# Optimization experiments

Hardware: AMD Instinct MI355X
Metric: run time of the kernel (lower is better)

## Reference

```python
import jax, jax.numpy as jnp
import numpy as np

B, M, N = 32, 16, 256        # problems, constraints, items
P = M * N                    # nodes per problem graph (4096)
NODES = B * P                # 131072
E = 2_097_152                # edges (avg degree 16)
F_IN = 16
H = 128                      # n_hidden[0..5], n_hidden[7]
H6 = 256                     # n_hidden[6]


def setup_inputs() -> dict:
    key = jax.random.key(0)
    ks = jax.random.split(key, 24)
    nrm = lambda k, shape: jax.random.normal(k, shape, jnp.float32) * 0.05
    inp = {}
    inp["G"] = jax.random.normal(ks[0], (NODES, F_IN), jnp.float32)
    inp["edge_index"] = jax.random.randint(ks[1], (2, E), 0, NODES)
    inp["edge_weight"] = jax.random.uniform(ks[2], (E,), jnp.float32)
    inp["edge_attribute"] = jax.random.normal(ks[3], (E, 1), jnp.float32)  # unused, kept for API parity
    inp["value_var_solutions"] = jax.random.randint(ks[4], (B, P), 0, 2).astype(jnp.int32)
    inp["item_values"] = jax.random.uniform(ks[5], (B, N), jnp.float32)
    # learned parameters
    inp["W_emb1"], inp["b_emb1"] = nrm(ks[6], (F_IN, H)), jnp.zeros((H,), jnp.float32)
    inp["W_emb2"], inp["b_emb2"] = nrm(ks[7], (H, H)), jnp.zeros((H,), jnp.float32)
    for i, t in enumerate(("c1", "c2")):  # GatedGraphConv(H, num_layers=2) x2
        inp[f"{t}_W"]  = nrm(ks[8 + 3 * i], (2, H, H))
        inp[f"{t}_wi"] = nrm(ks[9 + 3 * i], (3 * H, H))
        inp[f"{t}_wh"] = nrm(ks[10 + 3 * i], (3 * H, H))
        inp[f"{t}_bi"] = jnp.zeros((3 * H,), jnp.float32)
        inp[f"{t}_bh"] = jnp.zeros((3 * H,), jnp.float32)
    inp["W_g1"], inp["b_g1"] = nrm(ks[14], (H, H)), jnp.zeros((H,), jnp.float32)
    inp["W_g2"], inp["b_g2"] = nrm(ks[15], (H, H)), jnp.zeros((H,), jnp.float32)
    inp["W_l1"], inp["b_l1"] = nrm(ks[16], (2 * H, H6)), jnp.zeros((H6,), jnp.float32)
    inp["W_l2"], inp["b_l2"] = nrm(ks[17], (H6, H)), jnp.zeros((H,), jnp.float32)
    inp["W_l3"], inp["b_l3"] = nrm(ks[18], (H, 1)), jnp.zeros((1,), jnp.float32)
    return inp


def _gru_cell(m, h, wi, wh, bi, bh):
    # torch.nn.GRUCell with gate order (r, z, n)
    gi = m @ wi.T + bi
    gh = h @ wh.T + bh
    ir, iz, inn = jnp.split(gi, 3, axis=-1)
    hr, hz, hn = jnp.split(gh, 3, axis=-1)
    r = jax.nn.sigmoid(ir + hr)
    z = jax.nn.sigmoid(iz + hz)
    n = jnp.tanh(inn + r * hn)
    return (1.0 - z) * n + z * h


def _gated_graph_conv(x, src, dst, ew, W, wi, wh, bi, bh):
    # PyG GatedGraphConv: for each layer, m_i = sum_{j->i} ew * (x_j @ W_l); x = GRU(m, x)
    nnodes = x.shape[0]
    for l in range(W.shape[0]):
        msg = (x @ W[l])[src] * ew[:, None]          # [E, H]
        agg = jax.ops.segment_sum(msg, dst, num_segments=nnodes)
        x = _gru_cell(agg, x, wi, wh, bi, bh)
    return x


def reference(G, edge_index, edge_weight, edge_attribute, value_var_solutions, item_values,
              W_emb1, b_emb1, W_emb2, b_emb2,
              c1_W, c1_wi, c1_wh, c1_bi, c1_bh,
              c2_W, c2_wi, c2_wh, c2_bi, c2_bh,
              W_g1, b_g1, W_g2, b_g2,
              W_l1, b_l1, W_l2, b_l2, W_l3, b_l3):
    src, dst = edge_index[0], edge_index[1]
    x = jax.nn.relu(G @ W_emb1 + b_emb1)
    x = jax.nn.relu(x @ W_emb2 + b_emb2)
    x = jax.nn.relu(_gated_graph_conv(x, src, dst, edge_weight, c1_W, c1_wi, c1_wh, c1_bi, c1_bh))
    x = jax.nn.relu(_gated_graph_conv(x, src, dst, edge_weight, c2_W, c2_wi, c2_wh, c2_bi, c2_bh))
    x = jax.nn.relu(x @ W_g1 + b_g1)
    x = x @ W_g2 + b_g2                              # [NODES, H]
    # ragged per-graph mean pool + broadcast-concat (all graphs same size -> reshape)
    xg = x.reshape(B, P, H)
    ge = xg.mean(axis=1, keepdims=True)              # [B, 1, H] graph embedding
    u = jnp.concatenate([xg, jnp.broadcast_to(ge, xg.shape)], axis=-1)  # [B, P, 2H]
    u = jax.nn.relu(u @ W_l1 + b_l1)
    u = jax.nn.relu(u @ W_l2 + b_l2)
    u = (u @ W_l3 + b_l3)[..., 0]                    # [B, P]
    # bound: dx[j,i] = sol[0,i] - sol[j,i]; bound = u.dx + sum_i val[i]*sol[0,i]
    sol = value_var_solutions.reshape(B, M, N).astype(u.dtype)
    dx = sol[:, :1, :] - sol                         # [B, M, N]
    bounds = (jnp.einsum('bp,bp->b', u, dx.reshape(B, P))
              + jnp.einsum('bn,bn->b', item_values, sol[:, 0, :]))
    return bounds
```

## Files before the change

### kernel.cpp

```cpp
#include <hip/hip_runtime.h>

#define NODES   131072
#define EDGES   2097152
#define H       128
#define NB      32
#define PP      4096

typedef short bf16x8 __attribute__((ext_vector_type(8)));
typedef float f32x4  __attribute__((ext_vector_type(4)));
typedef float f32x2  __attribute__((ext_vector_type(2)));
typedef unsigned short u16;

#define RZE 65536
#define AIE 16384
#define AHE 16384
#define LYRE (RZE + AIE + AHE)

#define CAPP 18432

__global__ __launch_bounds__(128) void gnn_pinit(int* __restrict__ pcur) {
  pcur[threadIdx.x] = threadIdx.x * CAPP;
}

#define B1_BLOCKS 256
#define B1_TILES  4
__global__ __launch_bounds__(256) void gnn_bin1(const int* __restrict__ src, const int* __restrict__ dst,
                                                const float* __restrict__ ew, int* __restrict__ pcur,
                                                uint2* __restrict__ stage) {
  __shared__ int hist[128];
  __shared__ int pbase[128];
  const int tid = threadIdx.x;
  for (int t = 0; t < B1_TILES; ++t) {
    if (tid < 128) hist[tid] = 0;
    __syncthreads();
    const int ebase = blockIdx.x * (B1_TILES * 2048) + t * 2048;
    int parts[8], ranks[8];
    uint2 recs[8];
#pragma unroll
    for (int i = 0; i < 8; ++i) {
      int e = ebase + i * 256 + tid;
      int d = dst[e];
      int s = src[e];
      float w = ew[e];
      int wq = (int)fminf(w * 32768.f + 0.5f, 32767.f);
      parts[i] = d >> 10;
      recs[i].x = ((unsigned)s << 15) | (unsigned)wq;
      recs[i].y = (unsigned)d;
      ranks[i] = atomicAdd(&hist[parts[i]], 1);
    }
    __syncthreads();
    if (tid < 128) {
      int c = hist[tid];
      pbase[tid] = c ? atomicAdd(&pcur[tid], c) : 0;
    }
    __syncthreads();
#pragma unroll
    for (int i = 0; i < 8; ++i)
      stage[pbase[parts[i]] + ranks[i]] = recs[i];
    __syncthreads();
  }
}

__global__ __launch_bounds__(256) void gnn_bin2(const uint2* __restrict__ stage,
                                                const int* __restrict__ pcur,
                                                int* __restrict__ rowptr,
                                                unsigned* __restrict__ epack) {
  __shared__ int h[1024];
  __shared__ int ws[256];
  __shared__ int pc[128];
  __shared__ int gb_s;
  const int tid = threadIdx.x;
  const int p = blockIdx.x;
  const int node0 = p << 10;
  const int s0 = p * CAPP;
  const int cnt = pcur[p] - s0;
#pragma unroll
  for (int i = 0; i < 4; ++i) h[i * 256 + tid] = 0;
  if (tid < 128) pc[tid] = pcur[tid] - tid * CAPP;
  __syncthreads();
  for (int r = tid; r < cnt; r += 256)
    atomicAdd(&h[(int)stage[s0 + r].y - node0], 1);
  if (tid == 0) {
    int s = 0;
    for (int i = 0; i < p; ++i) s += pc[i];
    gb_s = s;
  }
  __syncthreads();
  const int gbase = gb_s;
  int a0 = h[tid * 4 + 0], a1 = h[tid * 4 + 1], a2 = h[tid * 4 + 2], a3 = h[tid * 4 + 3];
  int s1 = a0 + a1, s2 = s1 + a2, s3 = s2 + a3;
  ws[tid] = s3;
  __syncthreads();
  for (int o = 1; o < 256; o <<= 1) {
    int u = (tid >= o) ? ws[tid - o] : 0;
    __syncthreads();
    ws[tid] += u;
    __syncthreads();
  }
  int eb = gbase + (tid ? ws[tid - 1] : 0);
  int4 rp;
  rp.x = eb; rp.y = eb + a0; rp.z = eb + s1; rp.w = eb + s2;
  *(int4*)(rowptr + node0 + tid * 4) = rp;
  h[tid * 4 + 0] = rp.x; h[tid * 4 + 1] = rp.y; h[tid * 4 + 2] = rp.z; h[tid * 4 + 3] = rp.w;
  if (p == 127 && tid == 255) rowptr[NODES] = EDGES;
  __syncthreads();
  for (int r = tid; r < cnt; r += 256) {
    uint2 q = stage[s0 + r];
    int pos = atomicAdd(&h[(int)q.y - node0], 1);
    epack[pos] = q.x;
  }
}

__device__ __forceinline__ unsigned gnn_pack2bf(float a, float b) {
  union { float f; unsigned u; } x, y; x.f = a; y.f = b;
  unsigned ua = (x.u + 0x7FFFu + ((x.u >> 16) & 1u)) >> 16;
  unsigned ub = (y.u + 0x7FFFu + ((y.u >> 16) & 1u)) >> 16;
  return ua | (ub << 16);
}

__device__ __forceinline__ u16 gnn_f2bf(float a) {
  union { float f; unsigned u; } x; x.f = a;
  return (u16)((x.u + 0x7FFFu + ((x.u >> 16) & 1u)) >> 16);
}

__device__ __forceinline__ float gnn_bf2f(u16 h) {
  union { unsigned u; float f; } x; x.u = ((unsigned)h) << 16; return x.f;
}

__device__ __forceinline__ unsigned char gnn_f2fp8(float v) {
  return (unsigned char)(__builtin_amdgcn_cvt_pk_fp8_f32(v, v, 0, false) & 0xFF);
}

template<bool HI>
__device__ __forceinline__ unsigned gnn_bf2fp8pk(unsigned pv, unsigned old) {
  union { unsigned u; float f; } lo, hi;
  lo.u = pv << 16; hi.u = pv & 0xFFFF0000u;
  return __builtin_amdgcn_cvt_pk_fp8_f32(lo.f, hi.f, old, HI);
}

__device__ __forceinline__ float gnn_sig(float x)  { return 1.f / (1.f + __expf(-x)); }
__device__ __forceinline__ float gnn_tanh(float x) { return 1.f - 2.f / (1.f + __expf(2.f * x)); }

__global__ __launch_bounds__(256) void gnn_agg(const unsigned char* __restrict__ X8,
                                               const int* __restrict__ rowptr,
                                               const unsigned* __restrict__ epack,
                                               u16* __restrict__ T) {
  const int tid = threadIdx.x;
  const int wave = tid >> 6, lane = tid & 63;
  const int g = lane >> 4, s = lane & 15;
  const unsigned soff = (unsigned)(s << 3);
  const int node = blockIdx.x * 16 + wave * 4 + g;
  const int e1 = rowptr[node + 1];
  const int e0 = rowptr[node];
  float acc[8];
#pragma unroll
  for (int c = 0; c < 8; ++c) acc[c] = 0.f;

  for (int it = e0; __any(it < e1); it += 8) {
    unsigned qv[8];
#pragma unroll
    for (int j = 0; j < 8; ++j) {
      int t = it + j;
      t = t < e1 ? t : e1 - 1;
      t = t < 0 ? 0 : t;
      qv[j] = epack[t];
    }
    uint2 pv[8];
#pragma unroll
    for (int j = 0; j < 8; ++j)
      pv[j] = *(const uint2*)(X8 + ((((qv[j] >> 15) << 7)) | soff));
#pragma unroll
    for (int j = 0; j < 8; ++j) {
      float w = (it + j) < e1 ? (float)(qv[j] & 0x7FFFu) : 0.f;
      f32x2 f01 = __builtin_amdgcn_cvt_pk_f32_fp8(pv[j].x, false);
      f32x2 f23 = __builtin_amdgcn_cvt_pk_f32_fp8(pv[j].x, true);
      f32x2 f45 = __builtin_amdgcn_cvt_pk_f32_fp8(pv[j].y, false);
      f32x2 f67 = __builtin_amdgcn_cvt_pk_f32_fp8(pv[j].y, true);
      acc[0] = fmaf(w, f01.x, acc[0]);  acc[1] = fmaf(w, f01.y, acc[1]);
      acc[2] = fmaf(w, f23.x, acc[2]);  acc[3] = fmaf(w, f23.y, acc[3]);
      acc[4] = fmaf(w, f45.x, acc[4]);  acc[5] = fmaf(w, f45.y, acc[5]);
      acc[6] = fmaf(w, f67.x, acc[6]);  acc[7] = fmaf(w, f67.y, acc[7]);
    }
  }

  const float sc = 1.f / 32768.f;
  uint4 o;
  o.x = gnn_pack2bf(acc[0] * sc, acc[1] * sc);
  o.y = gnn_pack2bf(acc[2] * sc, acc[3] * sc);
  o.z = gnn_pack2bf(acc[4] * sc, acc[5] * sc);
  o.w = gnn_pack2bf(acc[6] * sc, acc[7] * sc);
  *(uint4*)(T + (long)node * H + s * 8) = o;
}

__global__ __launch_bounds__(384) void gnn_prep(const float* __restrict__ c1W, const float* __restrict__ c1wi,
                                                const float* __restrict__ c2W, const float* __restrict__ c2wi,
                                                const float* __restrict__ wh1, const float* __restrict__ wh2,
                                                float* __restrict__ Wc, float* __restrict__ whT) {
  if (blockIdx.x < 512) {
    __shared__ float wrow[128];
    int l = blockIdx.x >> 7, k = blockIdx.x & 127, j = threadIdx.x;
    const float* Wl = (l < 2 ? c1W : c2W) + (l & 1) * 128 * 128;
    const float* wi = l < 2 ? c1wi : c2wi;
    if (j < 128) wrow[j] = Wl[k * 128 + j];
    __syncthreads();
    float acc = 0.f;
    for (int m = 0; m < 128; ++m) acc = fmaf(wrow[m], wi[j * 128 + m], acc);
    Wc[(long)l * 49152 + k * 384 + j] = acc;
  } else {
    int bb = blockIdx.x - 512;
    int c = bb >> 7, k = bb & 127, j = threadIdx.x;
    const float* wh = c ? wh2 : wh1;
    whT[((long)c * 128 + k) * 384 + j] = wh[j * 128 + k];
  }
}

template<int K>
__device__ __forceinline__ void gnn_stage_bf(const u16* __restrict__ A, long row0,
                                             u16* lds, int tid) {
  constexpr int CH = K / 8;
#pragma unroll
  for (int it = 0; it < (64 * CH) / 256; ++it) {
    int c = it * 256 + tid;
    int row = c / CH, ktq = c % CH;
    uint4 v = *(const uint4*)(A + (row0 + row) * K + ktq * 8);
    int slot = ktq * 64 + (row ^ (ktq & 7));
    *(uint4*)(lds + slot * 8) = v;
  }
}

template<int K>
__device__ __forceinline__ void gnn_stage32(const u16* __restrict__ A, long row0,
                                            u16* lds, int tid) {
  constexpr int CH = K / 8;
#pragma unroll
  for (int it = 0; it < (32 * CH) / 256; ++it) {
    int c = it * 256 + tid;
    int row = c / CH, ktq = c % CH;
    uint4 v = *(const uint4*)(A + (row0 + row) * K + ktq * 8);
    int slot = ktq * 32 + (row ^ (ktq & 7));
    *(uint4*)(lds + slot * 8) = v;
  }
}

__device__ __forceinline__ bf16x8 gnn_afrag(const u16* lds, int rt, int ktq, int l16) {
  int slot = ktq * 64 + ((rt * 16 + l16) ^ (ktq & 7));
  return *(const bf16x8*)(lds + slot * 8);
}

__device__ __forceinline__ bf16x8 gnn_afrag32(const u16* lds, int rt, int ktq, int l16) {
  int slot = ktq * 32 + ((rt * 16 + l16) ^ (ktq & 7));
  return *(const bf16x8*)(lds + slot * 8);
}

__device__ __forceinline__ bf16x8 gnn_bfrag(const u16* __restrict__ pk,
                                            int ct, int kt, int KT, int lane) {
  return *(const bf16x8*)(pk + (((long)(ct * KT + kt)) * 64 + lane) * 8);
}

__device__ __forceinline__ void gnn_lds_put(u16* lds, int row, int col, float v) {
  int kq = col >> 3, of = col & 7;
  lds[(kq * 64 + (row ^ (kq & 7))) * 8 + of] = gnn_f2bf(v);
}

__device__ __forceinline__ float gnn_lds_get(const u16* lds, int row, int col) {
  int kq = col >> 3, of = col & 7;
  return gnn_bf2f(lds[(kq * 64 + (row ^ (kq & 7))) * 8 + of]);
}

__device__ __forceinline__ float gnn_lds_get32(const u16* lds, int row, int col) {
  int kq = col >> 3, of = col & 7;
  return gnn_bf2f(lds[(kq * 32 + (row ^ (kq & 7))) * 8 + of]);
}

__device__ __forceinline__ void gnn_pack_body(const float* __restrict__ W0, const float* __restrict__ W1,
                                              int ksplit, int LD, int coff, int KT, int b, int lane,
                                              u16* __restrict__ dst) {
  int kt = b % KT, ct = b / KT;
  int col = ct * 16 + (lane & 15) + coff;
  int kb = kt * 32 + ((lane >> 4) & 3) * 8;
  u16 h[8];
#pragma unroll
  for (int j = 0; j < 8; ++j) {
    int k = kb + j;
    float v = (k < ksplit) ? W0[(long)k * LD + col] : W1[(long)(k - ksplit) * LD + col];
    h[j] = gnn_f2bf(v);
  }
  uint4 o;
  o.x = (unsigned)h[0] | ((unsigned)h[1] << 16);
  o.y = (unsigned)h[2] | ((unsigned)h[3] << 16);
  o.z = (unsigned)h[4] | ((unsigned)h[5] << 16);
  o.w = (unsigned)h[6] | ((unsigned)h[7] << 16);
  ((uint4*)dst)[(long)b * 64 + lane] = o;
}

__global__ __launch_bounds__(64) void gnn_pack(const float* __restrict__ Wc, const float* __restrict__ whT,
                                               const float* __restrict__ We2, const float* __restrict__ Wg1,
                                               const float* __restrict__ Wg2, const float* __restrict__ Wl1,
                                               const float* __restrict__ Wl2, u16* __restrict__ pk) {
  int lane = threadIdx.x;
  if (blockIdx.x < 768) {
    int l = blockIdx.x / 192, r = blockIdx.x % 192;
    const float* Wcl = Wc + (long)l * 49152;
    const float* whl = whT + (long)(l >> 1) * 49152;
    u16* base = pk + (long)l * LYRE;
    if (r < 128)      gnn_pack_body(Wcl, whl, 128, 384, 0,   8, r,       lane, base);
    else if (r < 160) gnn_pack_body(Wcl, Wcl, 128, 384, 256, 4, r - 128, lane, base + RZE);
    else              gnn_pack_body(whl, whl, 128, 384, 256, 4, r - 160, lane, base + RZE + AIE);
  } else {
    int b = blockIdx.x - 768;
    u16* pe2 = pk + 4 * LYRE;
    if (b < 32)       gnn_pack_body(We2, We2, 128, 128, 0, 4, b,       lane, pe2);
    else if (b < 64)  gnn_pack_body(Wg1, Wg1, 128, 128, 0, 4, b - 32,  lane, pe2 + 16384);
    else if (b < 96)  gnn_pack_body(Wg2, Wg2, 128, 128, 0, 4, b - 64,  lane, pe2 + 32768);
    else if (b < 160) gnn_pack_body(Wl1, Wl1, 128, 256, 0, 4, b - 96,  lane, pe2 + 49152);
    else              gnn_pack_body(Wl2, Wl2, 256, 128, 0, 8, b - 160, lane, pe2 + 81920);
  }
}

__global__ __launch_bounds__(256) void gnn_emb(const float* __restrict__ G, const float* __restrict__ W1,
                                               const float* __restrict__ b1,
                                               const u16* __restrict__ pk2, const float* __restrict__ b2,
                                               u16* __restrict__ C, unsigned char* __restrict__ C8) {
  __shared__ u16 As[64 * 128];
  __shared__ float AsT[16][68];
  __shared__ float Ws[16][132];
  const int tid = threadIdx.x;
  const int lane = tid & 63, wave = tid >> 6;
  const int quad = lane >> 4, l16 = lane & 15;
  const long row0 = (long)blockIdx.x * 64;

  {
    const int lr  = tid >> 2;
    const int lk4 = (tid & 3) * 4;
    const int wk  = tid >> 4;
    const int wj4 = (tid & 15) * 4;
    float4 a = *(const float4*)(G + (row0 + lr) * 16 + lk4);
    AsT[lk4 + 0][lr] = a.x; AsT[lk4 + 1][lr] = a.y; AsT[lk4 + 2][lr] = a.z; AsT[lk4 + 3][lr] = a.w;
    float4 w0 = *(const float4*)(W1 + (long)wk * 128 + wj4);
    float4 w1 = *(const float4*)(W1 + (long)wk * 128 + 64 + wj4);
    *(float4*)(&Ws[wk][wj4]) = w0;
    *(float4*)(&Ws[wk][64 + wj4]) = w1;
    __syncthreads();

    const int tx = tid & 15, ty = tid >> 4;
    float acc0[16], acc1[16];
#pragma unroll
    for (int i = 0; i < 16; ++i) { acc0[i] = 0.f; acc1[i] = 0.f; }
#pragma unroll
    for (int k = 0; k < 16; ++k) {
      float4 av  = *(const float4*)(&AsT[k][ty * 4]);
      float4 wv0 = *(const float4*)(&Ws[k][tx * 4]);
      float4 wv1 = *(const float4*)(&Ws[k][64 + tx * 4]);
#pragma unroll
      for (int i = 0; i < 4; ++i) {
        float av_i = (i == 0) ? av.x : (i == 1) ? av.y : (i == 2) ? av.z : av.w;
        acc0[i * 4 + 0] = fmaf(av_i, wv0.x, acc0[i * 4 + 0]);
        acc0[i * 4 + 1] = fmaf(av_i, wv0.y, acc0[i * 4 + 1]);
        acc0[i * 4 + 2] = fmaf(av_i, wv0.z, acc0[i * 4 + 2]);
        acc0[i * 4 + 3] = fmaf(av_i, wv0.w, acc0[i * 4 + 3]);
        acc1[i * 4 + 0] = fmaf(av_i, wv1.x, acc1[i * 4 + 0]);
        acc1[i * 4 + 1] = fmaf(av_i, wv1.y, acc1[i * 4 + 1]);
        acc1[i * 4 + 2] = fmaf(av_i, wv1.z, acc1[i * 4 + 2]);
        acc1[i * 4 + 3] = fmaf(av_i, wv1.w, acc1[i * 4 + 3]);
      }
    }
#pragma unroll
    for (int i = 0; i < 4; ++i) {
      int row = ty * 4 + i;
#pragma unroll
      for (int j = 0; j < 4; ++j) {
        int c0 = tx * 4 + j;
        gnn_lds_put(As, row, c0,      fmaxf(acc0[i * 4 + j] + b1[c0], 0.f));
        gnn_lds_put(As, row, c0 + 64, fmaxf(acc1[i * 4 + j] + b1[c0 + 64], 0.f));
      }
    }
  }
  __syncthreads();

  f32x4 zero4 = {0.f, 0.f, 0.f, 0.f};
  f32x4 acc[4][2];
#pragma unroll
  for (int rt = 0; rt < 4; ++rt)
#pragma unroll
    for (int ct = 0; ct < 2; ++ct) acc[rt][ct] = zero4;
#pragma unroll
  for (int kt = 0; kt < 4; ++kt) {
    int ktq = kt * 4 + quad;
    bf16x8 af[4];
#pragma unroll
    for (int rt = 0; rt < 4; ++rt) af[rt] = gnn_afrag(As, rt, ktq, l16);
#pragma unroll
    for (int ct = 0; ct < 2; ++ct) {
      bf16x8 bf = gnn_bfrag(pk2, wave * 2 + ct, kt, 4, lane);
#pragma unroll
      for (int rt = 0; rt < 4; ++rt)
        acc[rt][ct] = __builtin_amdgcn_mfma_f32_16x16x32_bf16(af[rt], bf, acc[rt][ct], 0, 0, 0);
    }
  }
#pragma unroll
  for (int ct = 0; ct < 2; ++ct) {
    int col = (wave * 2 + ct) * 16 + l16;
    float bv = b2[col];
#pragma unroll
    for (int rt = 0; rt < 4; ++rt) {
      long row = row0 + rt * 16 + quad * 4;
#pragma unroll
      for (int r = 0; r < 4; ++r) {
        float v = fmaxf(acc[rt][ct][r] + bv, 0.f);
        C[(row + r) * H + col] = gnn_f2bf(v);
        C8[(row + r) * H + col] = gnn_f2fp8(v);
      }
    }
  }
}

#define OSTR 136

template<int RELU>
__global__ __launch_bounds__(256, 3) void gnn_mgru(const u16* __restrict__ T, const u16* __restrict__ X,
                                                   const u16* __restrict__ pkRZ,
                                                   const u16* __restrict__ pkAI,
                                                   const u16* __restrict__ pkAH,
                                                   const float* __restrict__ bi, const float* __restrict__ bh,
                                                   u16* __restrict__ Y,
                                                   unsigned char* __restrict__ Y8) {
  __shared__ u16 Ts[32 * OSTR];
  __shared__ u16 Xs[32 * 128];
  const int tid = threadIdx.x;
  const int lane = tid & 63, wave = tid >> 6;
  const int quad = lane >> 4, l16 = lane & 15;
  const long row0 = (long)blockIdx.x * 32;
  gnn_stage32<128>(T, row0, Ts, tid);
  gnn_stage32<128>(X, row0, Xs, tid);

  float brz[2], bzz[2], bin_[2], bhn[2];
#pragma unroll
  for (int c = 0; c < 2; ++c) {
    int col = (wave * 2 + c) * 16 + l16;
    brz[c]  = bi[col] + bh[col];
    bzz[c]  = bi[128 + col] + bh[128 + col];
    bin_[c] = bi[256 + col];
    bhn[c]  = bh[256 + col];
  }
  __syncthreads();

  f32x4 zero4 = {0.f, 0.f, 0.f, 0.f};
  f32x4 g1[2][2], g2[2][2];

#pragma unroll
  for (int rt = 0; rt < 2; ++rt)
#pragma unroll
    for (int c = 0; c < 2; ++c) g1[rt][c] = zero4;
#pragma unroll
  for (int kt = 0; kt < 4; ++kt) {
    int ktq = kt * 4 + quad;
    bf16x8 tf[2], xf[2];
#pragma unroll
    for (int rt = 0; rt < 2; ++rt) { tf[rt] = gnn_afrag32(Ts, rt, ktq, l16); xf[rt] = gnn_afrag32(Xs, rt, ktq, l16); }
#pragma unroll
    for (int c = 0; c < 2; ++c) {
      int ct = wave * 2 + c;
      bf16x8 bRT = gnn_bfrag(pkRZ, ct, kt,     8, lane);
      bf16x8 bRX = gnn_bfrag(pkRZ, ct, kt + 4, 8, lane);
#pragma unroll
      for (int rt = 0; rt < 2; ++rt) {
        g1[rt][c] = __builtin_amdgcn_mfma_f32_16x16x32_bf16(tf[rt], bRT, g1[rt][c], 0, 0, 0);
        g1[rt][c] = __builtin_amdgcn_mfma_f32_16x16x32_bf16(xf[rt], bRX, g1[rt][c], 0, 0, 0);
      }
    }
  }
#pragma unroll
  for (int rt = 0; rt < 2; ++rt)
#pragma unroll
    for (int c = 0; c < 2; ++c)
#pragma unroll
      for (int r = 0; r < 4; ++r)
        g1[rt][c][r] = gnn_sig(g1[rt][c][r] + brz[c]);

#pragma unroll
  for (int rt = 0; rt < 2; ++rt)
#pragma unroll
    for (int c = 0; c < 2; ++c) g2[rt][c] = zero4;
#pragma unroll
  for (int kt = 0; kt < 4; ++kt) {
    int ktq = kt * 4 + quad;
    bf16x8 xf[2];
#pragma unroll
    for (int rt = 0; rt < 2; ++rt) xf[rt] = gnn_afrag32(Xs, rt, ktq, l16);
#pragma unroll
    for (int c = 0; c < 2; ++c) {
      bf16x8 bAH = gnn_bfrag(pkAH, wave * 2 + c, kt, 4, lane);
#pragma unroll
      for (int rt = 0; rt < 2; ++rt)
        g2[rt][c] = __builtin_amdgcn_mfma_f32_16x16x32_bf16(xf[rt], bAH, g2[rt][c], 0, 0, 0);
    }
  }
#pragma unroll
  for (int rt = 0; rt < 2; ++rt)
#pragma unroll
    for (int c = 0; c < 2; ++c)
#pragma unroll
      for (int r = 0; r < 4; ++r)
        g1[rt][c][r] = g1[rt][c][r] * (g2[rt][c][r] + bhn[c]);

#pragma unroll
  for (int rt = 0; rt < 2; ++rt)
#pragma unroll
    for (int c = 0; c < 2; ++c) g2[rt][c] = zero4;
#pragma unroll
  for (int kt = 0; kt < 4; ++kt) {
    int ktq = kt * 4 + quad;
    bf16x8 tf[2];
#pragma unroll
    for (int rt = 0; rt < 2; ++rt) tf[rt] = gnn_afrag32(Ts, rt, ktq, l16);
#pragma unroll
    for (int c = 0; c < 2; ++c) {
      bf16x8 bAI = gnn_bfrag(pkAI, wave * 2 + c, kt, 4, lane);
#pragma unroll
      for (int rt = 0; rt < 2; ++rt)
        g2[rt][c] = __builtin_amdgcn_mfma_f32_16x16x32_bf16(tf[rt], bAI, g2[rt][c], 0, 0, 0);
    }
  }
#pragma unroll
  for (int rt = 0; rt < 2; ++rt)
#pragma unroll
    for (int c = 0; c < 2; ++c)
#pragma unroll
      for (int r = 0; r < 4; ++r)
        g1[rt][c][r] = gnn_tanh(g2[rt][c][r] + bin_[c] + g1[rt][c][r]);

#pragma unroll
  for (int rt = 0; rt < 2; ++rt)
#pragma unroll
    for (int c = 0; c < 2; ++c) g2[rt][c] = zero4;
#pragma unroll
  for (int kt = 0; kt < 4; ++kt) {
    int ktq = kt * 4 + quad;
    bf16x8 tf[2], xf[2];
#pragma unroll
    for (int rt = 0; rt < 2; ++rt) { tf[rt] = gnn_afrag32(Ts, rt, ktq, l16); xf[rt] = gnn_afrag32(Xs, rt, ktq, l16); }
#pragma unroll
    for (int c = 0; c < 2; ++c) {
      int ct = wave * 2 + c;
      bf16x8 bZT = gnn_bfrag(pkRZ, 8 + ct, kt,     8, lane);
      bf16x8 bZX = gnn_bfrag(pkRZ, 8 + ct, kt + 4, 8, lane);
#pragma unroll
      for (int rt = 0; rt < 2; ++rt) {
        g2[rt][c] = __builtin_amdgcn_mfma_f32_16x16x32_bf16(tf[rt], bZT, g2[rt][c], 0, 0, 0);
        g2[rt][c] = __builtin_amdgcn_mfma_f32_16x16x32_bf16(xf[rt], bZX, g2[rt][c], 0, 0, 0);
      }
    }
  }

  float yv[2][2][4];
#pragma unroll
  for (int rt = 0; rt < 2; ++rt)
#pragma unroll
    for (int c = 0; c < 2; ++c) {
      int col = (wave * 2 + c) * 16 + l16;
      int rowl = rt * 16 + quad * 4;
#pragma unroll
      for (int r = 0; r < 4; ++r) {
        float z = gnn_sig(g2[rt][c][r] + bzz[c]);
        float h = gnn_lds_get32(Xs, rowl + r, col);
        float v = (1.f - z) * g1[rt][c][r] + z * h;
        if (RELU) v = fmaxf(v, 0.f);
        yv[rt][c][r] = v;
      }
    }
  __syncthreads();
#pragma unroll
  for (int rt = 0; rt < 2; ++rt)
#pragma unroll
    for (int c = 0; c < 2; ++c) {
      int col = (wave * 2 + c) * 16 + l16;
      int rowl = rt * 16 + quad * 4;
#pragma unroll
      for (int r = 0; r < 4; ++r)
        Ts[(rowl + r) * OSTR + col] = gnn_f2bf(yv[rt][c][r]);
    }
  __syncthreads();
  {
    const int orow = tid >> 3;
    const int oc = (tid & 7) * 16;
    const u16* src = Ts + orow * OSTR + oc;
    uint4 a = *(const uint4*)(src);
    uint4 b = *(const uint4*)(src + 8);
    u16* yd = Y + (row0 + orow) * H + oc;
    *(uint4*)(yd) = a;
    *(uint4*)(yd + 8) = b;
    if (Y8) {
      uint4 o8;
      o8.x = gnn_bf2fp8pk<true>(a.y, gnn_bf2fp8pk<false>(a.x, 0));
      o8.y = gnn_bf2fp8pk<true>(a.w, gnn_bf2fp8pk<false>(a.z, 0));
      o8.z = gnn_bf2fp8pk<true>(b.y, gnn_bf2fp8pk<false>(b.x, 0));
      o8.w = gnn_bf2fp8pk<true>(b.w, gnn_bf2fp8pk<false>(b.z, 0));
      *(uint4*)(Y8 + (row0 + orow) * H + oc) = o8;
    }
  }
}

__global__ __launch_bounds__(256) void gnn_g1g2(const u16* __restrict__ A,
                                                const u16* __restrict__ pk1, const float* __restrict__ b1,
                                                const u16* __restrict__ pk2, const float* __restrict__ b2,
                                                u16* __restrict__ C, float* __restrict__ ge) {
  __shared__ u16 As[64 * 128];
  __shared__ u16 Ys[64 * 128];
  const int tid = threadIdx.x;
  const int lane = tid & 63, wave = tid >> 6;
  const int quad = lane >> 4, l16 = lane & 15;
  const long row0 = (long)blockIdx.x * 64;
  gnn_stage_bf<128>(A, row0, As, tid);
  __syncthreads();

  f32x4 zero4 = {0.f, 0.f, 0.f, 0.f};
  f32x4 acc[4][2];
#pragma unroll
  for (int rt = 0; rt < 4; ++rt)
#pragma unroll
    for (int ct = 0; ct < 2; ++ct) acc[rt][ct] = zero4;
#pragma unroll
  for (int kt = 0; kt < 4; ++kt) {
    int ktq = kt * 4 + quad;
    bf16x8 af[4];
#pragma unroll
    for (int rt = 0; rt < 4; ++rt) af[rt] = gnn_afrag(As, rt, ktq, l16);
#pragma unroll
    for (int ct = 0; ct < 2; ++ct) {
      bf16x8 bf = gnn_bfrag(pk1, wave * 2 + ct, kt, 4, lane);
#pragma unroll
      for (int rt = 0; rt < 4; ++rt)
        acc[rt][ct] = __builtin_amdgcn_mfma_f32_16x16x32_bf16(af[rt], bf, acc[rt][ct], 0, 0, 0);
    }
  }
#pragma unroll
  for (int ct = 0; ct < 2; ++ct) {
    int col = (wave * 2 + ct) * 16 + l16;
    float bv = b1[col];
#pragma unroll
    for (int rt = 0; rt < 4; ++rt) {
      int rowl = rt * 16 + quad * 4;
#pragma unroll
      for (int r = 0; r < 4; ++r)
        gnn_lds_put(Ys, rowl + r, col, fmaxf(acc[rt][ct][r] + bv, 0.f));
    }
  }
  __syncthreads();

  f32x4 acc2[4][2];
#pragma unroll
  for (int rt = 0; rt < 4; ++rt)
#pragma unroll
    for (int ct = 0; ct < 2; ++ct) acc2[rt][ct] = zero4;
#pragma unroll
  for (int kt = 0; kt < 4; ++kt) {
    int ktq = kt * 4 + quad;
    bf16x8 af[4];
#pragma unroll
    for (int rt = 0; rt < 4; ++rt) af[rt] = gnn_afrag(Ys, rt, ktq, l16);
#pragma unroll
    for (int ct = 0; ct < 2; ++ct) {
      bf16x8 bf = gnn_bfrag(pk2, wave * 2 + ct, kt, 4, lane);
#pragma unroll
      for (int rt = 0; rt < 4; ++rt)
        acc2[rt][ct] = __builtin_amdgcn_mfma_f32_16x16x32_bf16(af[rt], bf, acc2[rt][ct], 0, 0, 0);
    }
  }
  float psum[2];
#pragma unroll
  for (int ct = 0; ct < 2; ++ct) {
    int col = (wave * 2 + ct) * 16 + l16;
    float bv = b2[col];
    float cs = 0.f;
#pragma unroll
    for (int rt = 0; rt < 4; ++rt) {
      long row = row0 + rt * 16 + quad * 4;
#pragma unroll
      for (int r = 0; r < 4; ++r) {
        float v = acc2[rt][ct][r] + bv;
        cs += v;
        C[(row + r) * H + col] = gnn_f2bf(v);
      }
    }
    psum[ct] = cs;
  }
  const int b = (int)(row0 >> 12);
#pragma unroll
  for (int ct = 0; ct < 2; ++ct) {
    float v = psum[ct];
    v += __shfl_xor(v, 16);
    v += __shfl_xor(v, 32);
    if (quad == 0) {
      int col = (wave * 2 + ct) * 16 + l16;
      atomicAdd(&ge[b * H + col], v);
    }
  }
}

__global__ __launch_bounds__(256) void gnn_l1l2(const u16* __restrict__ A,
                                                const u16* __restrict__ pk1, const float* __restrict__ gb,
                                                const u16* __restrict__ pk2, const float* __restrict__ b2,
                                                u16* __restrict__ C) {
  __shared__ u16 As[64 * 128];
  __shared__ u16 Us[64 * 256];
  const int tid = threadIdx.x;
  const int lane = tid & 63, wave = tid >> 6;
  const int quad = lane >> 4, l16 = lane & 15;
  const long row0 = (long)blockIdx.x * 64;
  gnn_stage_bf<128>(A, row0, As, tid);
  __syncthreads();

  f32x4 zero4 = {0.f, 0.f, 0.f, 0.f};
  {
    f32x4 acc[4][4];
#pragma unroll
    for (int rt = 0; rt < 4; ++rt)
#pragma unroll
      for (int ct = 0; ct < 4; ++ct) acc[rt][ct] = zero4;
#pragma unroll
    for (int kt = 0; kt < 4; ++kt) {
      int ktq = kt * 4 + quad;
      bf16x8 af[4];
#pragma unroll
      for (int rt = 0; rt < 4; ++rt) af[rt] = gnn_afrag(As, rt, ktq, l16);
#pragma unroll
      for (int ct = 0; ct < 4; ++ct) {
        bf16x8 bf = gnn_bfrag(pk1, wave * 4 + ct, kt, 4, lane);
#pragma unroll
        for (int rt = 0; rt < 4; ++rt)
          acc[rt][ct] = __builtin_amdgcn_mfma_f32_16x16x32_bf16(af[rt], bf, acc[rt][ct], 0, 0, 0);
      }
    }
    const float* bp = gb + (row0 >> 12) * 256;
#pragma unroll
    for (int ct = 0; ct < 4; ++ct) {
      int col = (wave * 4 + ct) * 16 + l16;
      float bv = bp[col];
#pragma unroll
      for (int rt = 0; rt < 4; ++rt) {
        int rowl = rt * 16 + quad * 4;
#pragma unroll
        for (int r = 0; r < 4; ++r)
          gnn_lds_put(Us, rowl + r, col, fmaxf(acc[rt][ct][r] + bv, 0.f));
      }
    }
  }
  __syncthreads();

  f32x4 acc2[4][2];
#pragma unroll
  for (int rt = 0; rt < 4; ++rt)
#pragma unroll
    for (int ct = 0; ct < 2; ++ct) acc2[rt][ct] = zero4;
#pragma unroll
  for (int kt = 0; kt < 8; ++kt) {
    int ktq = kt * 4 + quad;
    bf16x8 af[4];
#pragma unroll
    for (int rt = 0; rt < 4; ++rt) af[rt] = gnn_afrag(Us, rt, ktq, l16);
#pragma unroll
    for (int ct = 0; ct < 2; ++ct) {
      bf16x8 bf = gnn_bfrag(pk2, wave * 2 + ct, kt, 8, lane);
#pragma unroll
      for (int rt = 0; rt < 4; ++rt)
        acc2[rt][ct] = __builtin_amdgcn_mfma_f32_16x16x32_bf16(af[rt], bf, acc2[rt][ct], 0, 0, 0);
    }
  }
#pragma unroll
  for (int ct = 0; ct < 2; ++ct) {
    int col = (wave * 2 + ct) * 16 + l16;
    float bv = b2[col];
#pragma unroll
    for (int rt = 0; rt < 4; ++rt) {
      long row = row0 + rt * 16 + quad * 4;
#pragma unroll
      for (int r = 0; r < 4; ++r)
        C[(row + r) * H + col] = gnn_f2bf(fmaxf(acc2[rt][ct][r] + bv, 0.f));
    }
  }
}

__global__ __launch_bounds__(256) void gnn_gbias(const float* __restrict__ ge, const float* __restrict__ Wl1b,
                                                 const float* __restrict__ bl1, float* __restrict__ gb) {
  __shared__ float g[128];
  int b = blockIdx.x, t = threadIdx.x;
  if (t < 128) g[t] = ge[b * H + t] * (1.f / 4096.f);
  __syncthreads();
  float acc = bl1[t];
  for (int k = 0; k < 128; ++k) acc = fmaf(g[k], Wl1b[k * 256 + t], acc);
  gb[b * 256 + t] = acc;
}

__global__ __launch_bounds__(256) void gnn_item(const float* __restrict__ iv, const int* __restrict__ vvs,
                                                float* __restrict__ out) {
  __shared__ float s[256];
  int b = blockIdx.x, t = threadIdx.x;
  float v = iv[b * 256 + t] * (float)vvs[(long)b * PP + t];
  s[t] = v; __syncthreads();
  for (int off = 128; off > 0; off >>= 1) {
    if (t < off) s[t] += s[t + off];
    __syncthreads();
  }
  if (t == 0) out[b] = s[0];
}

__global__ __launch_bounds__(256) void gnn_bound(const u16* __restrict__ U2, const float* __restrict__ wl3,
                                                 const float* __restrict__ bl3, const int* __restrict__ vvs,
                                                 float* __restrict__ out) {
  int tid = threadIdx.x;
  int wave = tid >> 6, lane = tid & 63;
  int b = blockIdx.x >> 6;
  long node0 = (long)blockIdx.x * 64 + wave * 16;
  float w0 = wl3[lane * 2], w1 = wl3[lane * 2 + 1];
  float bl = bl3[0];
  float acc = 0.f;
  for (int i = 0; i < 16; ++i) {
    long node = node0 + i;
    unsigned pv = *(const unsigned*)(U2 + node * H + lane * 2);
    union { unsigned u; float f; } lo, hi;
    lo.u = pv << 16; hi.u = pv & 0xFFFF0000u;
    float p = lo.f * w0 + hi.f * w1;
#pragma unroll
    for (int off = 32; off > 0; off >>= 1) p += __shfl_down(p, off);
    if (lane == 0) {
      int pp = (int)(node & (PP - 1));
      int m = pp >> 8, n = pp & 255;
      if (m != 0) {
        float dx = (float)(vvs[((long)b << 12) + n] - vvs[((long)b << 12) + pp]);
        acc += (p + bl) * dx;
      }
    }
  }
  __shared__ float s[4];
  if (lane == 0) s[wave] = acc;
  __syncthreads();
  if (tid == 0) atomicAdd(&out[b], s[0] + s[1] + s[2] + s[3]);
}

extern "C" void kernel_launch(void* const* d_in, const int* in_sizes, int n_in,
                              void* d_out, int out_size, void* d_ws, size_t ws_size,
                              hipStream_t stream) {
  const float* G      = (const float*)d_in[0];
  const int*   ei     = (const int*)d_in[1];
  const int*   esrc   = ei;
  const int*   edst   = ei + EDGES;
  const float* ew     = (const float*)d_in[2];
  const int*   vvs    = (const int*)d_in[4];
  const float* iv     = (const float*)d_in[5];
  const float* W_emb1 = (const float*)d_in[6];
  const float* b_emb1 = (const float*)d_in[7];
  const float* W_emb2 = (const float*)d_in[8];
  const float* b_emb2 = (const float*)d_in[9];
  const float* c1_W   = (const float*)d_in[10];
  const float* c1_wi  = (const float*)d_in[11];
  const float* c1_wh  = (const float*)d_in[12];
  const float* c1_bi  = (const float*)d_in[13];
  const float* c1_bh  = (const float*)d_in[14];
  const float* c2_W   = (const float*)d_in[15];
  const float* c2_wi  = (const float*)d_in[16];
  const float* c2_wh  = (const float*)d_in[17];
  const float* c2_bi  = (const float*)d_in[18];
  const float* c2_bh  = (const float*)d_in[19];
  const float* W_g1   = (const float*)d_in[20];
  const float* b_g1   = (const float*)d_in[21];
  const float* W_g2   = (const float*)d_in[22];
  const float* b_g2   = (const float*)d_in[23];
  const float* W_l1   = (const float*)d_in[24];
  const float* b_l1   = (const float*)d_in[25];
  const float* W_l2   = (const float*)d_in[26];
  const float* b_l2   = (const float*)d_in[27];
  const float* W_l3   = (const float*)d_in[28];
  const float* b_l3   = (const float*)d_in[29];
  float* out = (float*)d_out;
  (void)in_sizes; (void)n_in; (void)out_size; (void)ws_size;

  char* wsb = (char*)d_ws;
  size_t off = 0;
  auto carve = [&](size_t bytes) -> char* {
    char* p = wsb + off;
    off += (bytes + 255) & ~(size_t)255;
    return p;
  };
  u16*   xa     = (u16*)carve(sizeof(u16) * (size_t)NODES * H);
  u16*   xc     = (u16*)carve(sizeof(u16) * (size_t)NODES * H);
  u16*   tb     = (u16*)carve(sizeof(u16) * (size_t)NODES * H);
  float* Wc     = (float*)carve(sizeof(float) * 4 * H * 384);
  float* whT    = (float*)carve(sizeof(float) * 2 * H * 384);
  u16*   pk     = (u16*)carve(sizeof(u16) * 507904);
  int*   rowptr = (int*)carve(sizeof(int) * (NODES + 1));
  int*   pcur   = (int*)carve(sizeof(int) * 128);
  uint2* stage  = (uint2*)carve(sizeof(uint2) * (size_t)128 * CAPP);
  unsigned* epack = (unsigned*)carve(sizeof(unsigned) * EDGES);
  float* ge     = (float*)carve(sizeof(float) * NB * H);
  float* gb     = (float*)carve(sizeof(float) * NB * 256);

  unsigned char* X8 = (unsigned char*)stage;

  u16* pkRZ[4]; u16* pkAI[4]; u16* pkAH[4];
  for (int l = 0; l < 4; ++l) {
    pkRZ[l] = pk + (long)l * LYRE;
    pkAI[l] = pk + (long)l * LYRE + RZE;
    pkAH[l] = pk + (long)l * LYRE + RZE + AIE;
  }
  u16* pe2 = pk + 4 * LYRE;
  u16* pg1 = pe2 + 16384;
  u16* pg2 = pe2 + 32768;
  u16* pl1 = pe2 + 49152;
  u16* pl2 = pe2 + 81920;

  hipMemsetAsync(ge, 0, sizeof(float) * NB * H, stream);
  gnn_pinit<<<1, 128, 0, stream>>>(pcur);
  gnn_bin1<<<B1_BLOCKS, 256, 0, stream>>>(esrc, edst, ew, pcur, stage);
  gnn_bin2<<<128, 256, 0, stream>>>(stage, pcur, rowptr, epack);

  gnn_prep<<<768, 384, 0, stream>>>(c1_W, c1_wi, c2_W, c2_wi, c1_wh, c2_wh, Wc, whT);
  gnn_pack<<<992, 64, 0, stream>>>(Wc, whT, W_emb2, W_g1, W_g2, W_l1, W_l2, pk);

  gnn_emb<<<NODES / 64, 256, 0, stream>>>(G, W_emb1, b_emb1, pe2, b_emb2, xc, X8);

  gnn_agg<<<NODES / 16, 256, 0, stream>>>(X8, rowptr, epack, tb);
  gnn_mgru<0><<<NODES / 32, 256, 0, stream>>>(tb, xc, pkRZ[0], pkAI[0], pkAH[0], c1_bi, c1_bh, xa, X8);
  gnn_agg<<<NODES / 16, 256, 0, stream>>>(X8, rowptr, epack, tb);
  gnn_mgru<1><<<NODES / 32, 256, 0, stream>>>(tb, xa, pkRZ[1], pkAI[1], pkAH[1], c1_bi, c1_bh, xc, X8);

  gnn_agg<<<NODES / 16, 256, 0, stream>>>(X8, rowptr, epack, tb);
  gnn_mgru<0><<<NODES / 32, 256, 0, stream>>>(tb, xc, pkRZ[2], pkAI[2], pkAH[2], c2_bi, c2_bh, xa, X8);
  gnn_agg<<<NODES / 16, 256, 0, stream>>>(X8, rowptr, epack, tb);
  gnn_mgru<1><<<NODES / 32, 256, 0, stream>>>(tb, xa, pkRZ[3], pkAI[3], pkAH[3], c2_bi, c2_bh, xc, nullptr);

  gnn_g1g2<<<NODES / 64, 256, 0, stream>>>(xc, pg1, b_g1, pg2, b_g2, tb, ge);

  gnn_gbias<<<NB, 256, 0, stream>>>(ge, W_l1 + 128 * 256, b_l1, gb);

  gnn_l1l2<<<NODES / 64, 256, 0, stream>>>(tb, pl1, gb, pl2, b_l2, xa);

  gnn_item<<<NB, 256, 0, stream>>>(iv, vvs, out);
  gnn_bound<<<NODES / 64, 256, 0, stream>>>(xa, W_l3, b_l3, vvs, out);
}
```

Measured before the change: 705.5 us.

## Fuse tail kernels: graph bias into g1g2, bound into l1l2, init merged

Merges the memset, partition init and item-value reduction into a single init kernel. The graph-bias projection now runs inside the last g1g2 block, found with an atomic ticket, instead of a separate launch. The final 128-to-1 projection and bound reduction are folded into the l1l2 epilogue, so the [NODES,128] bf16 activation is never written and re-read. This removes several launches and a 32 MB write-plus-read, but the last-block pattern serialises the bias computation on one block.

```diff
diff --git a/kernel.cpp b/kernel.cpp
--- a/kernel.cpp
+++ b/kernel.cpp
@@ -18,8 +18,26 @@
 
 #define CAPP 18432
 
-__global__ __launch_bounds__(128) void gnn_pinit(int* __restrict__ pcur) {
-  pcur[threadIdx.x] = threadIdx.x * CAPP;
+__global__ __launch_bounds__(256) void gnn_init(int* __restrict__ pcur, int* __restrict__ ticket,
+                                                float* __restrict__ ge,
+                                                const float* __restrict__ iv, const int* __restrict__ vvs,
+                                                float* __restrict__ out) {
+  const int tid = threadIdx.x;
+  if (blockIdx.x == 0) {
+    if (tid < 128) pcur[tid] = tid * CAPP;
+    if (tid == 128) *ticket = 0;
+    for (int i = tid; i < NB * H; i += 256) ge[i] = 0.f;
+  } else {
+    __shared__ float s[256];
+    int b = blockIdx.x - 1;
+    float v = iv[b * 256 + tid] * (float)vvs[(long)b * PP + tid];
+    s[tid] = v; __syncthreads();
+    for (int off = 128; off > 0; off >>= 1) {
+      if (tid < off) s[tid] += s[tid + off];
+      __syncthreads();
+    }
+    if (tid == 0) out[b] = s[0];
+  }
 }
 
 #define B1_BLOCKS 256
@@ -603,7 +621,10 @@
 __global__ __launch_bounds__(256) void gnn_g1g2(const u16* __restrict__ A,
                                                 const u16* __restrict__ pk1, const float* __restrict__ b1,
                                                 const u16* __restrict__ pk2, const float* __restrict__ b2,
-                                                u16* __restrict__ C, float* __restrict__ ge) {
+                                                u16* __restrict__ C, float* __restrict__ ge,
+                                                int* __restrict__ ticket,
+                                                const float* __restrict__ Wl1b, const float* __restrict__ bl1,
+                                                float* __restrict__ gb) {
   __shared__ u16 As[64 * 128];
   __shared__ u16 Ys[64 * 128];
   const int tid = threadIdx.x;
@@ -695,19 +716,39 @@
       atomicAdd(&ge[b * H + col], v);
     }
   }
+
+  __threadfence();
+  __syncthreads();
+  __shared__ int lastflag;
+  if (tid == 0) lastflag = (atomicAdd(ticket, 1) == (int)gridDim.x - 1) ? 1 : 0;
+  __syncthreads();
+  if (lastflag) {
+    __shared__ float g[128];
+    for (int bb = 0; bb < NB; ++bb) {
+      if (tid < 128) g[tid] = atomicAdd(&ge[bb * H + tid], 0.f) * (1.f / 4096.f);
+      __syncthreads();
+      float acc3 = bl1[tid];
+      for (int k = 0; k < 128; ++k) acc3 = fmaf(g[k], Wl1b[k * 256 + tid], acc3);
+      gb[bb * 256 + tid] = acc3;
+      __syncthreads();
+    }
+  }
 }
 
 __global__ __launch_bounds__(256) void gnn_l1l2(const u16* __restrict__ A,
                                                 const u16* __restrict__ pk1, const float* __restrict__ gb,
                                                 const u16* __restrict__ pk2, const float* __restrict__ b2,
-                                                u16* __restrict__ C) {
+                                                const float* __restrict__ wl3, const float* __restrict__ bl3,
+                                                const int* __restrict__ vvs, float* __restrict__ out) {
   __shared__ u16 As[64 * 128];
   __shared__ u16 Us[64 * 256];
+  __shared__ float rowsum[64];
   const int tid = threadIdx.x;
   const int lane = tid & 63, wave = tid >> 6;
   const int quad = lane >> 4, l16 = lane & 15;
   const long row0 = (long)blockIdx.x * 64;
   gnn_stage_bf<128>(A, row0, As, tid);
+  if (tid < 64) rowsum[tid] = 0.f;
   __syncthreads();
 
   f32x4 zero4 = {0.f, 0.f, 0.f, 0.f};
@@ -766,75 +807,42 @@
         acc2[rt][ct] = __builtin_amdgcn_mfma_f32_16x16x32_bf16(af[rt], bf, acc2[rt][ct], 0, 0, 0);
     }
   }
+
+  const int b = (int)(row0 >> 12);
+  float w3[2], bvv[2];
 #pragma unroll
   for (int ct = 0; ct < 2; ++ct) {
     int col = (wave * 2 + ct) * 16 + l16;
-    float bv = b2[col];
-#pragma unroll
-    for (int rt = 0; rt < 4; ++rt) {
-      long row = row0 + rt * 16 + quad * 4;
-#pragma unroll
-      for (int r = 0; r < 4; ++r)
-        C[(row + r) * H + col] = gnn_f2bf(fmaxf(acc2[rt][ct][r] + bv, 0.f));
-    }
-  }
-}
-
-__global__ __launch_bounds__(256) void gnn_gbias(const float* __restrict__ ge, const float* __restrict__ Wl1b,
-                                                 const float* __restrict__ bl1, float* __restrict__ gb) {
-  __shared__ float g[128];
-  int b = blockIdx.x, t = threadIdx.x;
-  if (t < 128) g[t] = ge[b * H + t] * (1.f / 4096.f);
-  __syncthreads();
-  float acc = bl1[t];
-  for (int k = 0; k < 128; ++k) acc = fmaf(g[k], Wl1b[k * 256 + t], acc);
-  gb[b * 256 + t] = acc;
-}
-
-__global__ __launch_bounds__(256) void gnn_item(const float* __restrict__ iv, const int* __restrict__ vvs,
-                                                float* __restrict__ out) {
-  __shared__ float s[256];
-  int b = blockIdx.x, t = threadIdx.x;
-  float v = iv[b * 256 + t] * (float)vvs[(long)b * PP + t];
-  s[t] = v; __syncthreads();
-  for (int off = 128; off > 0; off >>= 1) {
-    if (t < off) s[t] += s[t + off];
-    __syncthreads();
-  }
-  if (t == 0) out[b] = s[0];
-}
-
-__global__ __launch_bounds__(256) void gnn_bound(const u16* __restrict__ U2, const float* __restrict__ wl3,
-                                                 const float* __restrict__ bl3, const int* __restrict__ vvs,
-                                                 float* __restrict__ out) {
-  int tid = threadIdx.x;
-  int wave = tid >> 6, lane = tid & 63;
-  int b = blockIdx.x >> 6;
-  long node0 = (long)blockIdx.x * 64 + wave * 16;
-  float w0 = wl3[lane * 2], w1 = wl3[lane * 2 + 1];
-  float bl = bl3[0];
-  float acc = 0.f;
-  for (int i = 0; i < 16; ++i) {
-    long node = node0 + i;
-    unsigned pv = *(const unsigned*)(U2 + node * H + lane * 2);
-    union { unsigned u; float f; } lo, hi;
-    lo.u = pv << 16; hi.u = pv & 0xFFFF0000u;
-    float p = lo.f * w0 + hi.f * w1;
-#pragma unroll
-    for (int off = 32; off > 0; off >>= 1) p += __shfl_down(p, off);
-    if (lane == 0) {
-      int pp = (int)(node & (PP - 1));
-      int m = pp >> 8, n = pp & 255;
-      if (m != 0) {
-        float dx = (float)(vvs[((long)b << 12) + n] - vvs[((long)b << 12) + pp]);
-        acc += (p + bl) * dx;
-      }
-    }
-  }
-  __shared__ float s[4];
-  if (lane == 0) s[wave] = acc;
-  __syncthreads();
-  if (tid == 0) atomicAdd(&out[b], s[0] + s[1] + s[2] + s[3]);
+    w3[ct] = wl3[col];
+    bvv[ct] = b2[col];
+  }
+#pragma unroll
+  for (int rt = 0; rt < 4; ++rt) {
+#pragma unroll
+    for (int r = 0; r < 4; ++r) {
+      float part = fmaxf(acc2[rt][0][r] + bvv[0], 0.f) * w3[0]
+                 + fmaxf(acc2[rt][1][r] + bvv[1], 0.f) * w3[1];
+      part += __shfl_xor(part, 1);
+      part += __shfl_xor(part, 2);
+      part += __shfl_xor(part, 4);
+      part += __shfl_xor(part, 8);
+      if (l16 == 0) atomicAdd(&rowsum[rt * 16 + quad * 4 + r], part);
+    }
+  }
+  __syncthreads();
+  if (tid < 64) {
+    float p = rowsum[tid] + bl3[0];
+    int pp = (int)(row0 & 4095) + tid;
+    int m = pp >> 8, n = pp & 255;
+    float contrib = 0.f;
+    if (m != 0) {
+      float dx = (float)(vvs[((long)b << 12) + n] - vvs[((long)b << 12) + pp]);
+      contrib = p * dx;
+    }
+#pragma unroll
+    for (int off = 32; off > 0; off >>= 1) contrib += __shfl_down(contrib, off);
+    if (tid == 0) atomicAdd(&out[b], contrib);
+  }
 }
 
 extern "C" void kernel_launch(void* const* d_in, const int* in_sizes, int n_in,
@@ -889,6 +897,7 @@
   u16*   pk     = (u16*)carve(sizeof(u16) * 507904);
   int*   rowptr = (int*)carve(sizeof(int) * (NODES + 1));
   int*   pcur   = (int*)carve(sizeof(int) * 128);
+  int*   ticket = (int*)carve(sizeof(int) * 64);
   uint2* stage  = (uint2*)carve(sizeof(uint2) * (size_t)128 * CAPP);
   unsigned* epack = (unsigned*)carve(sizeof(unsigned) * EDGES);
   float* ge     = (float*)carve(sizeof(float) * NB * H);
@@ -908,8 +917,8 @@
   u16* pl1 = pe2 + 49152;
   u16* pl2 = pe2 + 81920;
 
-  hipMemsetAsync(ge, 0, sizeof(float) * NB * H, stream);
-  gnn_pinit<<<1, 128, 0, stream>>>(pcur);
+  gnn_init<<<NB + 1, 256, 0, stream>>>(pcur, ticket, ge, iv, vvs, out);
+
   gnn_bin1<<<B1_BLOCKS, 256, 0, stream>>>(esrc, edst, ew, pcur, stage);
   gnn_bin2<<<128, 256, 0, stream>>>(stage, pcur, rowptr, epack);
 
@@ -928,12 +937,8 @@
   gnn_agg<<<NODES / 16, 256, 0, stream>>>(X8, rowptr, epack, tb);
   gnn_mgru<1><<<NODES / 32, 256, 0, stream>>>(tb, xa, pkRZ[3], pkAI[3], pkAH[3], c2_bi, c2_bh, xc, nullptr);
 
-  gnn_g1g2<<<NODES / 64, 256, 0, stream>>>(xc, pg1, b_g1, pg2, b_g2, tb, ge);
-
-  gnn_gbias<<<NB, 256, 0, stream>>>(ge, W_l1 + 128 * 256, b_l1, gb);
-
-  gnn_l1l2<<<NODES / 64, 256, 0, stream>>>(tb, pl1, gb, pl2, b_l2, xa);
-
-  gnn_item<<<NB, 256, 0, stream>>>(iv, vvs, out);
-  gnn_bound<<<NODES / 64, 256, 0, stream>>>(xa, W_l3, b_l3, vvs, out);
-}
+  gnn_g1g2<<<NODES / 64, 256, 0, stream>>>(xc, pg1, b_g1, pg2, b_g2, tb, ge,
+                                           ticket, W_l1 + 128 * 256, b_l1, gb);
+
+  gnn_l1l2<<<NODES / 64, 256, 0, stream>>>(tb, pl1, gb, pl2, b_l2, W_l3, b_l3, vvs, out);
+}
```

New measurement: 1.018 ms. 44.4% more time.
